# Performance work log

Hardware: AMD Instinct MI355X
Metric: run time of the kernel (lower is better)

Reference implementation:

```python
import jax, jax.numpy as jnp
import numpy as np

B, T, S, PD = 512, 2048, 16, 4

def setup_inputs() -> dict:
    key = jax.random.key(0)
    ks = jax.random.split(key, 10)
    w = lambda k, sh: (jax.random.normal(k, sh, dtype=jnp.float32) * 0.1)
    return {
        'z': jax.random.normal(ks[0], (B, T, S), dtype=jnp.float32),
        'p': jax.random.normal(ks[1], (B, T, PD), dtype=jnp.float32),
        'mu0': jnp.zeros((B, S), dtype=jnp.float32),
        'P0': jnp.full((B, S), 0.1, dtype=jnp.float32),  # cfg['kf_P0']
        'Wq1': w(ks[2], (PD, 64)), 'bq1': jnp.zeros((64,), jnp.float32),
        'Wq2': w(ks[3], (64, S)),  'bq2': jnp.zeros((S,), jnp.float32),
        'Wr1': w(ks[4], (PD, 64)), 'br1': jnp.zeros((64,), jnp.float32),
        'Wr2': w(ks[5], (64, S)),  'br2': jnp.zeros((S,), jnp.float32),
        'Wg1': w(ks[6], (PD, 32)), 'bg1': jnp.zeros((32,), jnp.float32),
        'Wg2': w(ks[7], (32, 1)),  'bg2': jnp.zeros((1,), jnp.float32),
    }

def _mlp(x, W1, b1, W2, b2):
    return jax.nn.relu(x @ W1 + b1) @ W2 + b2

def reference(z, p, mu0, P0, Wq1, bq1, Wq2, bq2, Wr1, br1, Wr2, br2, Wg1, bg1, Wg2, bg2):
    # z: [B,T,S], p: [B,T,PD]; scan over time with batched Kalman state.
    zT = jnp.swapaxes(z, 0, 1)  # [T,B,S]
    pT = jnp.swapaxes(p, 0, 1)  # [T,B,PD]

    def step(carry, inp):
        mu, P = carry            # [B,S], [B,S]
        z_t, p_t = inp           # [B,S], [B,PD]
        Q_t = jax.nn.softplus(_mlp(p_t, Wq1, bq1, Wq2, bq2)) + 1e-8
        R_t = jax.nn.softplus(_mlp(p_t, Wr1, br1, Wr2, br2)) + 1e-8
        P_pred = P + Q_t
        K = jnp.clip(P_pred / (P_pred + R_t), 1e-6, 0.95)
        gamma_t = jax.nn.sigmoid(_mlp(p_t, Wg1, bg1, Wg2, bg2))  # [B,1] (scalar per sample)
        mu_new = mu + gamma_t * (K * (z_t - mu))
        P_new = (1.0 - K) * P_pred
        return (mu_new, P_new), mu_new

    (mu_f, P_f), mus = jax.lax.scan(step, (mu0, P0), (zT, pT))
    return jnp.swapaxes(mus, 0, 1)  # [B,T,S]
```

## Files before the change

kernel.cpp:

```cpp
#include <hip/hip_runtime.h>
#include <hip/hip_fp16.h>
#include <stdint.h>
#include <math.h>

#define KB 512
#define KT 2048
#define KS 16
#define KPD 4

typedef _Float16 f16;
typedef _Float16 f16x4v __attribute__((ext_vector_type(4)));
typedef _Float16 f16x8 __attribute__((ext_vector_type(8)));
typedef float f32x4 __attribute__((ext_vector_type(4)));

#define MFMA16(A, B, C) __builtin_amdgcn_mfma_f32_16x16x32_f16(A, B, C, 0, 0, 0)

__device__ __forceinline__ float softplus_f(float x) {
    float ax = fabsf(x);
    float e  = __expf(-ax);
    return fmaxf(x, 0.0f) + __logf(1.0f + e);
}
__device__ __forceinline__ float sigmoid_f(float x) {
    return __builtin_amdgcn_rcpf(1.0f + __expf(-x));
}
__device__ __forceinline__ float h2f_lo(uint32_t w) {
    return __half2float(__ushort_as_half((unsigned short)(w & 0xffffu)));
}
__device__ __forceinline__ float h2f_hi(uint32_t w) {
    return __half2float(__ushort_as_half((unsigned short)(w >> 16)));
}
__device__ __forceinline__ f16x8 zero8() {
    f16x8 v;
#pragma unroll
    for (int i = 0; i < 8; ++i) v[i] = (f16)0;
    return v;
}

#define HRS 168

__global__ __launch_bounds__(64) void mlp_kernel(
    const float* __restrict__ p,
    const float* __restrict__ Wq1, const float* __restrict__ bq1,
    const float* __restrict__ Wq2, const float* __restrict__ bq2,
    const float* __restrict__ Wr1, const float* __restrict__ br1,
    const float* __restrict__ Wr2, const float* __restrict__ br2,
    const float* __restrict__ Wg1, const float* __restrict__ bg1,
    const float* __restrict__ Wg2, const float* __restrict__ bg2,
    uint32_t* __restrict__ qr_ws, float* __restrict__ g_ws)
{
    __shared__ __align__(16) f16 Hl[2][16][HRS];
    __shared__ __align__(16) f16 Pl[64][4];

    const int l = threadIdx.x;
    const int g = l >> 4;
    const int c = l & 15;
    const int row0 = blockIdx.x * 64;
    const int b = row0 >> 11;
    const int t0 = row0 & (KT - 1);

    f16x8 fA1[10];
#pragma unroll
    for (int m = 0; m < 10; ++m) {
        const float* W = (m < 4) ? (Wq1 + m * 16)
                       : (m < 8) ? (Wr1 + (m - 4) * 16)
                                 : (Wg1 + (m - 8) * 16);
        const int ld = (m < 8) ? 64 : 32;
        float w0 = W[0 * ld + c], w1 = W[1 * ld + c],
              w2 = W[2 * ld + c], w3 = W[3 * ld + c];
        f16x8 a = zero8();
        if (g == 0) { a[0] = (f16)w0; a[1] = (f16)w1; a[2] = (f16)w2; a[3] = (f16)w3; }
        fA1[m] = a;
    }

    f16x8 fA2[5];
#pragma unroll
    for (int i = 0; i < 4; ++i) {
        const float* W = (i < 2) ? Wq2 : Wr2;
        const int kb = (i & 1) * 32;
        f16x8 a;
#pragma unroll
        for (int j = 0; j < 8; ++j) a[j] = (f16)W[(kb + g * 8 + j) * 16 + c];
        fA2[i] = a;
    }
    {
        f16x8 a = zero8();
        if (c == 0) {
#pragma unroll
            for (int j = 0; j < 8; ++j) a[j] = (f16)Wg2[g * 8 + j];
        }
        fA2[4] = a;
    }

    const float bQ0 = bq2[g * 4 + 0], bQ1 = bq2[g * 4 + 1],
                bQ2 = bq2[g * 4 + 2], bQ3 = bq2[g * 4 + 3];
    const float bR0 = br2[g * 4 + 0], bR1 = br2[g * 4 + 1],
                bR2 = br2[g * 4 + 2], bR3 = br2[g * 4 + 3];
    const float bG = bg2[0];

    {
        const float4 pv = *reinterpret_cast<const float4*>(p + (size_t)(row0 + l) * KPD);
        f16x4v v; v[0] = (f16)pv.x; v[1] = (f16)pv.y; v[2] = (f16)pv.z; v[3] = (f16)pv.w;
        *reinterpret_cast<f16x4v*>(&Pl[l][0]) = v;
    }
    asm volatile("s_waitcnt lgkmcnt(0)" ::: "memory");
    __builtin_amdgcn_sched_barrier(0);

    f16x8 fBP[4];
#pragma unroll
    for (int n = 0; n < 4; ++n) {
        f16x8 v = zero8();
        if (g == 0) {
            f16x4v q = *reinterpret_cast<const f16x4v*>(&Pl[n * 16 + c][0]);
            v[0] = q[0]; v[1] = q[1]; v[2] = q[2]; v[3] = q[3];
        }
        fBP[n] = v;
    }

    auto gemm1 = [&](int n, int buf) {
#pragma unroll
        for (int m = 0; m < 10; ++m) {
            const float* bs = (m < 4) ? (bq1 + m * 16)
                            : (m < 8) ? (br1 + (m - 4) * 16)
                                      : (bg1 + (m - 8) * 16);
            f32x4 acc;
            acc[0] = bs[g * 4 + 0]; acc[1] = bs[g * 4 + 1];
            acc[2] = bs[g * 4 + 2]; acc[3] = bs[g * 4 + 3];
            acc = MFMA16(fA1[m], fBP[n], acc);
            auto h01 = __builtin_amdgcn_cvt_pkrtz(fmaxf(acc[0], 0.f), fmaxf(acc[1], 0.f));
            auto h23 = __builtin_amdgcn_cvt_pkrtz(fmaxf(acc[2], 0.f), fmaxf(acc[3], 0.f));
            uint2 w;
            __builtin_memcpy(&w.x, &h01, 4);
            __builtin_memcpy(&w.y, &h23, 4);
            *reinterpret_cast<uint2*>(&Hl[buf][c][m * 16 + g * 4]) = w;
        }
    };

    auto gemm2 = [&](int n, int buf) {
        f16x8 fb0 = *reinterpret_cast<const f16x8*>(&Hl[buf][c][0 * 32 + g * 8]);
        f16x8 fb1 = *reinterpret_cast<const f16x8*>(&Hl[buf][c][1 * 32 + g * 8]);
        f16x8 fb2 = *reinterpret_cast<const f16x8*>(&Hl[buf][c][2 * 32 + g * 8]);
        f16x8 fb3 = *reinterpret_cast<const f16x8*>(&Hl[buf][c][3 * 32 + g * 8]);
        f16x8 fb4 = *reinterpret_cast<const f16x8*>(&Hl[buf][c][4 * 32 + g * 8]);

        f32x4 aq; aq[0] = bQ0; aq[1] = bQ1; aq[2] = bQ2; aq[3] = bQ3;
        aq = MFMA16(fA2[0], fb0, aq);
        aq = MFMA16(fA2[1], fb1, aq);
        f32x4 ar; ar[0] = bR0; ar[1] = bR1; ar[2] = bR2; ar[3] = bR3;
        ar = MFMA16(fA2[2], fb2, ar);
        ar = MFMA16(fA2[3], fb3, ar);
        f32x4 ag; ag[0] = 0.f; ag[1] = 0.f; ag[2] = 0.f; ag[3] = 0.f;
        ag = MFMA16(fA2[4], fb4, ag);

        uint32_t* qdst = qr_ws + ((size_t)b * KS + g * 4) * KT + t0 + n * 16 + c;
#pragma unroll
        for (int i = 0; i < 4; ++i) {
            float Qv = softplus_f(aq[i]) + 1e-8f;
            float Rv = softplus_f(ar[i]) + 1e-8f;
            auto pk = __builtin_amdgcn_cvt_pkrtz(Qv, Rv);
            uint32_t w; __builtin_memcpy(&w, &pk, 4);
            qdst[(size_t)i * KT] = w;
        }
        if (g == 0)
            g_ws[(size_t)b * KT + t0 + n * 16 + c] = sigmoid_f(ag[0] + bG);
    };

    gemm1(0, 0);
#pragma unroll
    for (int n = 0; n < 4; ++n) {
        if (n < 3) gemm1(n + 1, (n + 1) & 1);
        gemm2(n, n & 1);
    }
}

#define QT 512
#define NQ (KT / QT)
#define CL 8

__global__ __launch_bounds__(1024) void scan_kernel(
    const uint32_t* __restrict__ qr_ws, const float* __restrict__ g_ws,
    const float* __restrict__ z, const float* __restrict__ mu0,
    const float* __restrict__ P0, float* __restrict__ out)
{
    __shared__ float smem[QT * 17 + QT];
    float* zmu = smem;
    float* gl  = smem + QT * 17;

    const int b = blockIdx.x;
    const int tid = threadIdx.x;
    const int lane = tid & 63;
    const int s = tid >> 6;

    const uint32_t* qrow = qr_ws + (size_t)(b * KS + s) * KT;
    const float* zb = z + (size_t)b * KT * KS;
    const float* gb = g_ws + (size_t)b * KT;
    float* ob = out + (size_t)b * KT * KS;

    float P_q  = P0[b * KS + s];
    float mu_q = mu0[b * KS + s];

    for (int q = 0; q < NQ; ++q) {
        const int t0 = q * QT;

        {
            const float4* zq = reinterpret_cast<const float4*>(zb + (size_t)t0 * KS);
#pragma unroll
            for (int v = 0; v < 2; ++v) {
                int k = tid * 2 + v;
                float4 w = zq[k];
                int t = k >> 2, s0 = (k & 3) << 2;
                zmu[t * 17 + s0 + 0] = w.x;
                zmu[t * 17 + s0 + 1] = w.y;
                zmu[t * 17 + s0 + 2] = w.z;
                zmu[t * 17 + s0 + 3] = w.w;
            }
            if (tid < QT) gl[tid] = gb[t0 + tid];
        }
        __syncthreads();

        uint32_t qr[CL];
        {
            const uint4* qp = reinterpret_cast<const uint4*>(qrow + t0 + lane * CL);
            uint4 u0 = qp[0], u1 = qp[1];
            qr[0] = u0.x; qr[1] = u0.y; qr[2] = u0.z; qr[3] = u0.w;
            qr[4] = u1.x; qr[5] = u1.y; qr[6] = u1.z; qr[7] = u1.w;
        }
        float c00 = 1.f, c01 = 0.f, c10 = 0.f, c11 = 1.f;
#pragma unroll
        for (int i = 0; i < CL; ++i) {
            float Q = h2f_lo(qr[i]), R = h2f_hi(qr[i]);
            float ta = fmaf(Q, c10, c00);
            float tb = fmaf(Q, c11, c01);
            float n10 = fmaf(Q + R, c10, c00);
            float n11 = fmaf(Q + R, c11, c01);
            c00 = R * ta; c01 = R * tb; c10 = n10; c11 = n11;
        }
        float rn = __builtin_amdgcn_rcpf(c11);
        float ma = c00 * rn, mb = c01 * rn, mc = c10 * rn;

#pragma unroll
        for (int r = 0; r < 6; ++r) {
            const int d = 1 << r;
            float pa = __shfl_up(ma, d);
            float pb = __shfl_up(mb, d);
            float pc = __shfl_up(mc, d);
            float na = fmaf(ma, pa, mb * pc);
            float nb = fmaf(ma, pb, mb);
            float nc = fmaf(mc, pa, pc);
            float nd = fmaf(mc, pb, 1.f);
            float rr = __builtin_amdgcn_rcpf(nd);
            bool act = (lane >= d);
            ma = act ? na * rr : ma;
            mb = act ? nb * rr : mb;
            mc = act ? nc * rr : mc;
        }
        float ea = __shfl_up(ma, 1);
        float eb = __shfl_up(mb, 1);
        float ec = __shfl_up(mc, 1);
        if (lane == 0) { ea = 1.f; eb = 0.f; ec = 0.f; }
        float P = fmaf(ea, P_q, eb) * __builtin_amdgcn_rcpf(fmaf(ec, P_q, 1.f));

        float av[CL], bw[CL];
        float A = 1.f, Bv = 0.f;
#pragma unroll
        for (int i = 0; i < CL; ++i) {
            float Q = h2f_lo(qr[i]), R = h2f_hi(qr[i]);
            float Pp = P + Q;
            float K0 = Pp * __builtin_amdgcn_rcpf(Pp + R);
            float Kk = __builtin_amdgcn_fmed3f(K0, 1e-6f, 0.95f);
            int t = lane * CL + i;
            float g = gl[t];
            float gk = g * Kk;
            float zv = zmu[t * 17 + s];
            av[i] = 1.f - gk;
            bw[i] = gk * zv;
            P = fmaf(-Kk, Pp, Pp);
            A = A * av[i];
            Bv = fmaf(av[i], Bv, bw[i]);
        }
        float P_end = __shfl(P, 63);

#pragma unroll
        for (int r = 0; r < 6; ++r) {
            const int d = 1 << r;
            float pA = __shfl_up(A, d);
            float pB = __shfl_up(Bv, d);
            float nA = A * pA;
            float nB = fmaf(A, pB, Bv);
            bool act = (lane >= d);
            A  = act ? nA : A;
            Bv = act ? nB : Bv;
        }
        float eA = __shfl_up(A, 1);
        float eB = __shfl_up(Bv, 1);
        if (lane == 0) { eA = 1.f; eB = 0.f; }
        float mu = fmaf(eA, mu_q, eB);

        __syncthreads();

#pragma unroll
        for (int i = 0; i < CL; ++i) {
            mu = fmaf(av[i], mu, bw[i]);
            zmu[(lane * CL + i) * 17 + s] = mu;
        }
        float mu_end = __shfl(mu, 63);
        __syncthreads();

#pragma unroll
        for (int v = 0; v < 2; ++v) {
            int k = tid * 2 + v;
            int t = k >> 2, s0 = (k & 3) << 2;
            float4 w;
            w.x = zmu[t * 17 + s0 + 0];
            w.y = zmu[t * 17 + s0 + 1];
            w.z = zmu[t * 17 + s0 + 2];
            w.w = zmu[t * 17 + s0 + 3];
            *reinterpret_cast<float4*>(ob + (size_t)(t0 + t) * KS + s0) = w;
        }
        P_q  = P_end;
        mu_q = mu_end;
        __syncthreads();
    }
}

#define KTT 128
#define KNT (KT / KTT)
#define SROW (KS + 1)

__device__ __forceinline__ void mlp16(const float4 pv,
    const float* __restrict__ W1, const float* __restrict__ b1,
    const float* __restrict__ W2, const float* __restrict__ b2,
    float* __restrict__ acc)
{
#pragma unroll
    for (int j = 0; j < KS; ++j) acc[j] = b2[j];
#pragma unroll 4
    for (int k = 0; k < 64; ++k) {
        float hk = b1[k];
        hk = fmaf(pv.x, W1[k],       hk);
        hk = fmaf(pv.y, W1[64 + k],  hk);
        hk = fmaf(pv.z, W1[128 + k], hk);
        hk = fmaf(pv.w, W1[192 + k], hk);
        hk = fmaxf(hk, 0.0f);
#pragma unroll
        for (int j = 0; j < KS; ++j) acc[j] = fmaf(hk, W2[k * KS + j], acc[j]);
    }
}

__global__ __launch_bounds__(320, 2) void kalman_fused(
    const float* __restrict__ z, const float* __restrict__ p,
    const float* __restrict__ mu0, const float* __restrict__ P0,
    const float* __restrict__ Wq1, const float* __restrict__ bq1,
    const float* __restrict__ Wq2, const float* __restrict__ bq2,
    const float* __restrict__ Wr1, const float* __restrict__ br1,
    const float* __restrict__ Wr2, const float* __restrict__ br2,
    const float* __restrict__ Wg1, const float* __restrict__ bg1,
    const float* __restrict__ Wg2, const float* __restrict__ bg2,
    float* __restrict__ out)
{
    __shared__ float sQ[2][KTT][SROW];
    __shared__ float sR[2][KTT][SROW];
    __shared__ float sZf[2][KTT][KS];
    __shared__ float sGf[2][KTT];

    const int b = blockIdx.x;
    const int tid = threadIdx.x;
    const float* __restrict__ zb = z + (size_t)b * KT * KS;
    const float* __restrict__ pb = p + (size_t)b * KT * KPD;
    float* __restrict__ outb = out + (size_t)b * KT * KS;

    const bool is_mlp = (tid < 256);

    auto do_mlp_tile = [&](int tile, int buf) {
        const int tt = tid & (KTT - 1);
        const int t = tile * KTT + tt;
        const float4 pv = *reinterpret_cast<const float4*>(pb + (size_t)t * KPD);
        float acc[KS];
        if (tid < KTT) {
            mlp16(pv, Wq1, bq1, Wq2, bq2, acc);
#pragma unroll
            for (int j = 0; j < KS; ++j)
                sQ[buf][tt][j] = softplus_f(acc[j]) + 1e-8f;
            float ag = bg2[0];
#pragma unroll 8
            for (int k = 0; k < 32; ++k) {
                float hk = bg1[k];
                hk = fmaf(pv.x, Wg1[k],      hk);
                hk = fmaf(pv.y, Wg1[32 + k], hk);
                hk = fmaf(pv.z, Wg1[64 + k], hk);
                hk = fmaf(pv.w, Wg1[96 + k], hk);
                hk = fmaxf(hk, 0.0f);
                ag = fmaf(hk, Wg2[k], ag);
            }
            sGf[buf][tt] = sigmoid_f(ag);
        } else {
            mlp16(pv, Wr1, br1, Wr2, br2, acc);
#pragma unroll
            for (int j = 0; j < KS; ++j)
                sR[buf][tt][j] = softplus_f(acc[j]) + 1e-8f;
        }
        const float4* __restrict__ zt =
            reinterpret_cast<const float4*>(zb + (size_t)tile * KTT * KS);
        float4* __restrict__ zd = reinterpret_cast<float4*>(&sZf[buf][0][0]);
        zd[tid] = zt[tid];
        zd[tid + 256] = zt[tid + 256];
    };

    float mu = 0.0f, Pv = 0.0f;
    if (!is_mlp) {
        const int lane = tid - 256;
        if (lane < KS) {
            mu = mu0[(size_t)b * KS + lane];
            Pv = P0[(size_t)b * KS + lane];
        }
    }

    if (is_mlp) do_mlp_tile(0, 0);
    __syncthreads();

    for (int k = 0; k < KNT; ++k) {
        const int cur = k & 1;
        if (is_mlp) {
            if (k + 1 < KNT) do_mlp_tile(k + 1, cur ^ 1);
        } else {
            const int lane = tid - 256;
            if (lane < KS) {
                const int s = lane;
                for (int tt = 0; tt < KTT; ++tt) {
                    const float Ppred = Pv + sQ[cur][tt][s];
                    float Kk = Ppred * __builtin_amdgcn_rcpf(Ppred + sR[cur][tt][s]);
                    Kk = __builtin_amdgcn_fmed3f(Kk, 1e-6f, 0.95f);
                    mu = fmaf(sGf[cur][tt] * Kk, sZf[cur][tt][s] - mu, mu);
                    Pv = fmaf(-Kk, Ppred, Ppred);
                    outb[(size_t)(k * KTT + tt) * KS + s] = mu;
                }
            }
        }
        __syncthreads();
    }
}

extern "C" void kernel_launch(void* const* d_in, const int* in_sizes, int n_in,
                              void* d_out, int out_size, void* d_ws, size_t ws_size,
                              hipStream_t stream) {
    const float* z   = (const float*)d_in[0];
    const float* p   = (const float*)d_in[1];
    const float* mu0 = (const float*)d_in[2];
    const float* P0  = (const float*)d_in[3];
    const float* Wq1 = (const float*)d_in[4];
    const float* bq1 = (const float*)d_in[5];
    const float* Wq2 = (const float*)d_in[6];
    const float* bq2 = (const float*)d_in[7];
    const float* Wr1 = (const float*)d_in[8];
    const float* br1 = (const float*)d_in[9];
    const float* Wr2 = (const float*)d_in[10];
    const float* br2 = (const float*)d_in[11];
    const float* Wg1 = (const float*)d_in[12];
    const float* bg1 = (const float*)d_in[13];
    const float* Wg2 = (const float*)d_in[14];
    const float* bg2 = (const float*)d_in[15];
    float* out = (float*)d_out;

    const size_t QR_BYTES = (size_t)KB * KS * KT * 4;
    const size_t G_BYTES  = (size_t)KB * KT * 4;

    if (ws_size >= QR_BYTES + G_BYTES) {
        uint32_t* qr_ws = (uint32_t*)d_ws;
        float* g_ws = (float*)((char*)d_ws + QR_BYTES);
        hipLaunchKernelGGL(mlp_kernel, dim3((KB * KT) / 64), dim3(64), 0, stream,
                           p, Wq1, bq1, Wq2, bq2, Wr1, br1, Wr2, br2,
                           Wg1, bg1, Wg2, bg2, qr_ws, g_ws);
        hipLaunchKernelGGL(scan_kernel, dim3(KB), dim3(1024), 0, stream,
                           qr_ws, g_ws, z, mu0, P0, out);
    } else {
        hipLaunchKernelGGL(kalman_fused, dim3(KB), dim3(320), 0, stream,
                           z, p, mu0, P0, Wq1, bq1, Wq2, bq2,
                           Wr1, br1, Wr2, br2, Wg1, bg1, Wg2, bg2, out);
    }
}
```

Measured before the change: 106.2 us.

## Fuse MFMA MLP and parallel-scan Kalman into one kernel via shared memory

Merges the separate MLP kernel and scan kernel into a single 512-thread kernel per batch. Each quarter of the sequence first has its Q/R/gamma values computed with MFMA and written to LDS, then two scans per wave run over it. This removes the global workspace round trip for Q/R/G (about 70 MB of writes and reads) and one kernel launch. In exchange, the MLP and scan phases are serialized inside each block, each wave now handles two states in sequence, and there are more barriers. The workspace-size fallback path is dropped.

```diff
diff --git a/kernel.cpp b/kernel.cpp
--- a/kernel.cpp
+++ b/kernel.cpp
@@ -7,9 +7,13 @@
 #define KT 2048
 #define KS 16
 #define KPD 4
+#define QT 512
+#define NQ (KT / QT)
+#define NWV 8
+#define HRS 168
+#define QSTR 516
 
 typedef _Float16 f16;
-typedef _Float16 f16x4v __attribute__((ext_vector_type(4)));
 typedef _Float16 f16x8 __attribute__((ext_vector_type(8)));
 typedef float f32x4 __attribute__((ext_vector_type(4)));
 
@@ -36,27 +40,34 @@
     return v;
 }
 
-#define HRS 168
-
-__global__ __launch_bounds__(64) void mlp_kernel(
-    const float* __restrict__ p,
+__global__ __launch_bounds__(512, 4) void kalman_one(
+    const float* __restrict__ z, const float* __restrict__ p,
+    const float* __restrict__ mu0, const float* __restrict__ P0,
     const float* __restrict__ Wq1, const float* __restrict__ bq1,
     const float* __restrict__ Wq2, const float* __restrict__ bq2,
     const float* __restrict__ Wr1, const float* __restrict__ br1,
     const float* __restrict__ Wr2, const float* __restrict__ br2,
     const float* __restrict__ Wg1, const float* __restrict__ bg1,
     const float* __restrict__ Wg2, const float* __restrict__ bg2,
-    uint32_t* __restrict__ qr_ws, float* __restrict__ g_ws)
+    float* __restrict__ out)
 {
-    __shared__ __align__(16) f16 Hl[2][16][HRS];
-    __shared__ __align__(16) f16 Pl[64][4];
-
-    const int l = threadIdx.x;
+    __shared__ __align__(16) uint32_t QRl[KS * QSTR];
+    __shared__ __align__(16) float    Gl[QT];
+    __shared__ __align__(16) uint32_t Ubuf[(NWV * KS * HRS) / 2];
+
+    const int tid = threadIdx.x;
+    const int wv = tid >> 6;
+    const int l = tid & 63;
     const int g = l >> 4;
     const int c = l & 15;
-    const int row0 = blockIdx.x * 64;
-    const int b = row0 >> 11;
-    const int t0 = row0 & (KT - 1);
+    const int b = blockIdx.x;
+
+    f16* __restrict__ Hw = reinterpret_cast<f16*>(Ubuf) + wv * (KS * HRS);
+    float* __restrict__ zmu = reinterpret_cast<float*>(Ubuf);
+
+    const float* __restrict__ zb = z + (size_t)b * KT * KS;
+    const float* __restrict__ pb = p + (size_t)b * KT * KPD;
+    float* __restrict__ ob = out + (size_t)b * KT * KS;
 
     f16x8 fA1[10];
 #pragma unroll
@@ -71,7 +82,6 @@
         if (g == 0) { a[0] = (f16)w0; a[1] = (f16)w1; a[2] = (f16)w2; a[3] = (f16)w3; }
         fA1[m] = a;
     }
-
     f16x8 fA2[5];
 #pragma unroll
     for (int i = 0; i < 4; ++i) {
@@ -90,122 +100,169 @@
         }
         fA2[4] = a;
     }
-
     const float bQ0 = bq2[g * 4 + 0], bQ1 = bq2[g * 4 + 1],
                 bQ2 = bq2[g * 4 + 2], bQ3 = bq2[g * 4 + 3];
     const float bR0 = br2[g * 4 + 0], bR1 = br2[g * 4 + 1],
                 bR2 = br2[g * 4 + 2], bR3 = br2[g * 4 + 3];
     const float bG = bg2[0];
 
-    {
-        const float4 pv = *reinterpret_cast<const float4*>(p + (size_t)(row0 + l) * KPD);
-        f16x4v v; v[0] = (f16)pv.x; v[1] = (f16)pv.y; v[2] = (f16)pv.z; v[3] = (f16)pv.w;
-        *reinterpret_cast<f16x4v*>(&Pl[l][0]) = v;
-    }
-    asm volatile("s_waitcnt lgkmcnt(0)" ::: "memory");
-    __builtin_amdgcn_sched_barrier(0);
-
-    f16x8 fBP[4];
-#pragma unroll
-    for (int n = 0; n < 4; ++n) {
-        f16x8 v = zero8();
-        if (g == 0) {
-            f16x4v q = *reinterpret_cast<const f16x4v*>(&Pl[n * 16 + c][0]);
-            v[0] = q[0]; v[1] = q[1]; v[2] = q[2]; v[3] = q[3];
-        }
-        fBP[n] = v;
-    }
-
-    auto gemm1 = [&](int n, int buf) {
-#pragma unroll
-        for (int m = 0; m < 10; ++m) {
-            const float* bs = (m < 4) ? (bq1 + m * 16)
-                            : (m < 8) ? (br1 + (m - 4) * 16)
-                                      : (bg1 + (m - 8) * 16);
-            f32x4 acc;
-            acc[0] = bs[g * 4 + 0]; acc[1] = bs[g * 4 + 1];
-            acc[2] = bs[g * 4 + 2]; acc[3] = bs[g * 4 + 3];
-            acc = MFMA16(fA1[m], fBP[n], acc);
-            auto h01 = __builtin_amdgcn_cvt_pkrtz(fmaxf(acc[0], 0.f), fmaxf(acc[1], 0.f));
-            auto h23 = __builtin_amdgcn_cvt_pkrtz(fmaxf(acc[2], 0.f), fmaxf(acc[3], 0.f));
-            uint2 w;
-            __builtin_memcpy(&w.x, &h01, 4);
-            __builtin_memcpy(&w.y, &h23, 4);
-            *reinterpret_cast<uint2*>(&Hl[buf][c][m * 16 + g * 4]) = w;
-        }
+    float muA = mu0[b * KS + wv],     PA = P0[b * KS + wv];
+    float muB = mu0[b * KS + wv + 8], PB = P0[b * KS + wv + 8];
+
+    auto scan_s = [&](int s, float& mu_q, float& P_q) {
+        uint32_t qr[8];
+        const uint32_t* qrow = QRl + (size_t)s * QSTR;
+#pragma unroll
+        for (int i = 0; i < 8; ++i) qr[i] = qrow[l * 8 + i];
+        float c00 = 1.f, c01 = 0.f, c10 = 0.f, c11 = 1.f;
+#pragma unroll
+        for (int i = 0; i < 8; ++i) {
+            float Q = h2f_lo(qr[i]), R = h2f_hi(qr[i]);
+            float ta = fmaf(Q, c10, c00);
+            float tb = fmaf(Q, c11, c01);
+            float n10 = fmaf(Q + R, c10, c00);
+            float n11 = fmaf(Q + R, c11, c01);
+            c00 = R * ta; c01 = R * tb; c10 = n10; c11 = n11;
+        }
+        float rn = __builtin_amdgcn_rcpf(c11);
+        float ma = c00 * rn, mb = c01 * rn, mc = c10 * rn;
+#pragma unroll
+        for (int r = 0; r < 6; ++r) {
+            const int d = 1 << r;
+            float pa = __shfl_up(ma, d);
+            float pbv = __shfl_up(mb, d);
+            float pc = __shfl_up(mc, d);
+            float na = fmaf(ma, pa, mb * pc);
+            float nb = fmaf(ma, pbv, mb);
+            float nc = fmaf(mc, pa, pc);
+            float nd = fmaf(mc, pbv, 1.f);
+            float rr = __builtin_amdgcn_rcpf(nd);
+            bool act = (l >= d);
+            ma = act ? na * rr : ma;
+            mb = act ? nb * rr : mb;
+            mc = act ? nc * rr : mc;
+        }
+        float ea = __shfl_up(ma, 1);
+        float eb = __shfl_up(mb, 1);
+        float ec = __shfl_up(mc, 1);
+        if (l == 0) { ea = 1.f; eb = 0.f; ec = 0.f; }
+        float P = fmaf(ea, P_q, eb) * __builtin_amdgcn_rcpf(fmaf(ec, P_q, 1.f));
+
+        float av[8], bw[8];
+        float A = 1.f, Bv = 0.f;
+#pragma unroll
+        for (int i = 0; i < 8; ++i) {
+            float Q = h2f_lo(qr[i]), R = h2f_hi(qr[i]);
+            float Pp = P + Q;
+            float K0 = Pp * __builtin_amdgcn_rcpf(Pp + R);
+            float Kk = __builtin_amdgcn_fmed3f(K0, 1e-6f, 0.95f);
+            int t = l * 8 + i;
+            float gv = Gl[t];
+            float gk = gv * Kk;
+            float zv = zmu[t * 17 + s];
+            av[i] = 1.f - gk;
+            bw[i] = gk * zv;
+            P = fmaf(-Kk, Pp, Pp);
+            A = A * av[i];
+            Bv = fmaf(av[i], Bv, bw[i]);
+        }
+        float P_end = __shfl(P, 63);
+#pragma unroll
+        for (int r = 0; r < 6; ++r) {
+            const int d = 1 << r;
+            float pA = __shfl_up(A, d);
+            float pB = __shfl_up(Bv, d);
+            float nA = A * pA;
+            float nB = fmaf(A, pB, Bv);
+            bool act = (l >= d);
+            A  = act ? nA : A;
+            Bv = act ? nB : Bv;
+        }
+        float eA = __shfl_up(A, 1);
+        float eB = __shfl_up(Bv, 1);
+        if (l == 0) { eA = 1.f; eB = 0.f; }
+        float mu = fmaf(eA, mu_q, eB);
+#pragma unroll
+        for (int i = 0; i < 8; ++i) {
+            mu = fmaf(av[i], mu, bw[i]);
+            zmu[(l * 8 + i) * 17 + s] = mu;
+        }
+        mu_q = __shfl(mu, 63);
+        P_q = P_end;
     };
 
-    auto gemm2 = [&](int n, int buf) {
-        f16x8 fb0 = *reinterpret_cast<const f16x8*>(&Hl[buf][c][0 * 32 + g * 8]);
-        f16x8 fb1 = *reinterpret_cast<const f16x8*>(&Hl[buf][c][1 * 32 + g * 8]);
-        f16x8 fb2 = *reinterpret_cast<const f16x8*>(&Hl[buf][c][2 * 32 + g * 8]);
-        f16x8 fb3 = *reinterpret_cast<const f16x8*>(&Hl[buf][c][3 * 32 + g * 8]);
-        f16x8 fb4 = *reinterpret_cast<const f16x8*>(&Hl[buf][c][4 * 32 + g * 8]);
-
-        f32x4 aq; aq[0] = bQ0; aq[1] = bQ1; aq[2] = bQ2; aq[3] = bQ3;
-        aq = MFMA16(fA2[0], fb0, aq);
-        aq = MFMA16(fA2[1], fb1, aq);
-        f32x4 ar; ar[0] = bR0; ar[1] = bR1; ar[2] = bR2; ar[3] = bR3;
-        ar = MFMA16(fA2[2], fb2, ar);
-        ar = MFMA16(fA2[3], fb3, ar);
-        f32x4 ag; ag[0] = 0.f; ag[1] = 0.f; ag[2] = 0.f; ag[3] = 0.f;
-        ag = MFMA16(fA2[4], fb4, ag);
-
-        uint32_t* qdst = qr_ws + ((size_t)b * KS + g * 4) * KT + t0 + n * 16 + c;
-#pragma unroll
-        for (int i = 0; i < 4; ++i) {
-            float Qv = softplus_f(aq[i]) + 1e-8f;
-            float Rv = softplus_f(ar[i]) + 1e-8f;
-            auto pk = __builtin_amdgcn_cvt_pkrtz(Qv, Rv);
-            uint32_t w; __builtin_memcpy(&w, &pk, 4);
-            qdst[(size_t)i * KT] = w;
-        }
-        if (g == 0)
-            g_ws[(size_t)b * KT + t0 + n * 16 + c] = sigmoid_f(ag[0] + bG);
-    };
-
-    gemm1(0, 0);
-#pragma unroll
-    for (int n = 0; n < 4; ++n) {
-        if (n < 3) gemm1(n + 1, (n + 1) & 1);
-        gemm2(n, n & 1);
-    }
-}
-
-#define QT 512
-#define NQ (KT / QT)
-#define CL 8
-
-__global__ __launch_bounds__(1024) void scan_kernel(
-    const uint32_t* __restrict__ qr_ws, const float* __restrict__ g_ws,
-    const float* __restrict__ z, const float* __restrict__ mu0,
-    const float* __restrict__ P0, float* __restrict__ out)
-{
-    __shared__ float smem[QT * 17 + QT];
-    float* zmu = smem;
-    float* gl  = smem + QT * 17;
-
-    const int b = blockIdx.x;
-    const int tid = threadIdx.x;
-    const int lane = tid & 63;
-    const int s = tid >> 6;
-
-    const uint32_t* qrow = qr_ws + (size_t)(b * KS + s) * KT;
-    const float* zb = z + (size_t)b * KT * KS;
-    const float* gb = g_ws + (size_t)b * KT;
-    float* ob = out + (size_t)b * KT * KS;
-
-    float P_q  = P0[b * KS + s];
-    float mu_q = mu0[b * KS + s];
-
     for (int q = 0; q < NQ; ++q) {
-        const int t0 = q * QT;
-
         {
-            const float4* zq = reinterpret_cast<const float4*>(zb + (size_t)t0 * KS);
-#pragma unroll
-            for (int v = 0; v < 2; ++v) {
-                int k = tid * 2 + v;
+            const int trow = q * QT + wv * 64;
+            const float4 pv = *reinterpret_cast<const float4*>(pb + (size_t)(trow + l) * KPD);
+
+            f16x8 fBP[4];
+#pragma unroll
+            for (int n = 0; n < 4; ++n) {
+                const int src = n * 16 + c;
+                float x = __shfl(pv.x, src);
+                float y = __shfl(pv.y, src);
+                float zz = __shfl(pv.z, src);
+                float w = __shfl(pv.w, src);
+                f16x8 v = zero8();
+                if (g == 0) { v[0] = (f16)x; v[1] = (f16)y; v[2] = (f16)zz; v[3] = (f16)w; }
+                fBP[n] = v;
+            }
+
+#pragma unroll
+            for (int n = 0; n < 4; ++n) {
+#pragma unroll
+                for (int m = 0; m < 10; ++m) {
+                    const float* bs = (m < 4) ? (bq1 + m * 16)
+                                    : (m < 8) ? (br1 + (m - 4) * 16)
+                                              : (bg1 + (m - 8) * 16);
+                    f32x4 acc;
+                    acc[0] = bs[g * 4 + 0]; acc[1] = bs[g * 4 + 1];
+                    acc[2] = bs[g * 4 + 2]; acc[3] = bs[g * 4 + 3];
+                    acc = MFMA16(fA1[m], fBP[n], acc);
+                    auto h01 = __builtin_amdgcn_cvt_pkrtz(fmaxf(acc[0], 0.f), fmaxf(acc[1], 0.f));
+                    auto h23 = __builtin_amdgcn_cvt_pkrtz(fmaxf(acc[2], 0.f), fmaxf(acc[3], 0.f));
+                    uint32_t w0, w1;
+                    __builtin_memcpy(&w0, &h01, 4);
+                    __builtin_memcpy(&w1, &h23, 4);
+                    *reinterpret_cast<uint32_t*>(&Hw[c * HRS + m * 16 + g * 4 + 0]) = w0;
+                    *reinterpret_cast<uint32_t*>(&Hw[c * HRS + m * 16 + g * 4 + 2]) = w1;
+                }
+                f16x8 fb0 = *reinterpret_cast<const f16x8*>(&Hw[c * HRS + 0 * 32 + g * 8]);
+                f16x8 fb1 = *reinterpret_cast<const f16x8*>(&Hw[c * HRS + 1 * 32 + g * 8]);
+                f16x8 fb2 = *reinterpret_cast<const f16x8*>(&Hw[c * HRS + 2 * 32 + g * 8]);
+                f16x8 fb3 = *reinterpret_cast<const f16x8*>(&Hw[c * HRS + 3 * 32 + g * 8]);
+                f16x8 fb4 = *reinterpret_cast<const f16x8*>(&Hw[c * HRS + 4 * 32 + g * 8]);
+
+                f32x4 aq; aq[0] = bQ0; aq[1] = bQ1; aq[2] = bQ2; aq[3] = bQ3;
+                aq = MFMA16(fA2[0], fb0, aq);
+                aq = MFMA16(fA2[1], fb1, aq);
+                f32x4 ar; ar[0] = bR0; ar[1] = bR1; ar[2] = bR2; ar[3] = bR3;
+                ar = MFMA16(fA2[2], fb2, ar);
+                ar = MFMA16(fA2[3], fb3, ar);
+                f32x4 ag; ag[0] = 0.f; ag[1] = 0.f; ag[2] = 0.f; ag[3] = 0.f;
+                ag = MFMA16(fA2[4], fb4, ag);
+
+                uint32_t* qdst = QRl + (size_t)(g * 4) * QSTR + wv * 64 + n * 16 + c;
+#pragma unroll
+                for (int i = 0; i < 4; ++i) {
+                    float Qv = softplus_f(aq[i]) + 1e-8f;
+                    float Rv = softplus_f(ar[i]) + 1e-8f;
+                    auto pk = __builtin_amdgcn_cvt_pkrtz(Qv, Rv);
+                    uint32_t w; __builtin_memcpy(&w, &pk, 4);
+                    qdst[(size_t)i * QSTR] = w;
+                }
+                if (g == 0)
+                    Gl[wv * 64 + n * 16 + c] = sigmoid_f(ag[0] + bG);
+            }
+        }
+        __syncthreads();
+
+        {
+            const float4* zq = reinterpret_cast<const float4*>(zb + (size_t)q * QT * KS);
+#pragma unroll
+            for (int v = 0; v < 4; ++v) {
+                int k = tid + 512 * v;
                 float4 w = zq[k];
                 int t = k >> 2, s0 = (k & 3) << 2;
                 zmu[t * 17 + s0 + 0] = w.x;
@@ -213,226 +270,25 @@
                 zmu[t * 17 + s0 + 2] = w.z;
                 zmu[t * 17 + s0 + 3] = w.w;
             }
-            if (tid < QT) gl[tid] = gb[t0 + tid];
         }
         __syncthreads();
 
-        uint32_t qr[CL];
+        scan_s(wv, muA, PA);
+        scan_s(wv + 8, muB, PB);
+        __syncthreads();
+
         {
-            const uint4* qp = reinterpret_cast<const uint4*>(qrow + t0 + lane * CL);
-            uint4 u0 = qp[0], u1 = qp[1];
-            qr[0] = u0.x; qr[1] = u0.y; qr[2] = u0.z; qr[3] = u0.w;
-            qr[4] = u1.x; qr[5] = u1.y; qr[6] = u1.z; qr[7] = u1.w;
-        }
-        float c00 = 1.f, c01 = 0.f, c10 = 0.f, c11 = 1.f;
-#pragma unroll
-        for (int i = 0; i < CL; ++i) {
-            float Q = h2f_lo(qr[i]), R = h2f_hi(qr[i]);
-            float ta = fmaf(Q, c10, c00);
-            float tb = fmaf(Q, c11, c01);
-            float n10 = fmaf(Q + R, c10, c00);
-            float n11 = fmaf(Q + R, c11, c01);
-            c00 = R * ta; c01 = R * tb; c10 = n10; c11 = n11;
-        }
-        float rn = __builtin_amdgcn_rcpf(c11);
-        float ma = c00 * rn, mb = c01 * rn, mc = c10 * rn;
-
-#pragma unroll
-        for (int r = 0; r < 6; ++r) {
-            const int d = 1 << r;
-            float pa = __shfl_up(ma, d);
-            float pb = __shfl_up(mb, d);
-            float pc = __shfl_up(mc, d);
-            float na = fmaf(ma, pa, mb * pc);
-            float nb = fmaf(ma, pb, mb);
-            float nc = fmaf(mc, pa, pc);
-            float nd = fmaf(mc, pb, 1.f);
-            float rr = __builtin_amdgcn_rcpf(nd);
-            bool act = (lane >= d);
-            ma = act ? na * rr : ma;
-            mb = act ? nb * rr : mb;
-            mc = act ? nc * rr : mc;
-        }
-        float ea = __shfl_up(ma, 1);
-        float eb = __shfl_up(mb, 1);
-        float ec = __shfl_up(mc, 1);
-        if (lane == 0) { ea = 1.f; eb = 0.f; ec = 0.f; }
-        float P = fmaf(ea, P_q, eb) * __builtin_amdgcn_rcpf(fmaf(ec, P_q, 1.f));
-
-        float av[CL], bw[CL];
-        float A = 1.f, Bv = 0.f;
-#pragma unroll
-        for (int i = 0; i < CL; ++i) {
-            float Q = h2f_lo(qr[i]), R = h2f_hi(qr[i]);
-            float Pp = P + Q;
-            float K0 = Pp * __builtin_amdgcn_rcpf(Pp + R);
-            float Kk = __builtin_amdgcn_fmed3f(K0, 1e-6f, 0.95f);
-            int t = lane * CL + i;
-            float g = gl[t];
-            float gk = g * Kk;
-            float zv = zmu[t * 17 + s];
-            av[i] = 1.f - gk;
-            bw[i] = gk * zv;
-            P = fmaf(-Kk, Pp, Pp);
-            A = A * av[i];
-            Bv = fmaf(av[i], Bv, bw[i]);
-        }
-        float P_end = __shfl(P, 63);
-
-#pragma unroll
-        for (int r = 0; r < 6; ++r) {
-            const int d = 1 << r;
-            float pA = __shfl_up(A, d);
-            float pB = __shfl_up(Bv, d);
-            float nA = A * pA;
-            float nB = fmaf(A, pB, Bv);
-            bool act = (lane >= d);
-            A  = act ? nA : A;
-            Bv = act ? nB : Bv;
-        }
-        float eA = __shfl_up(A, 1);
-        float eB = __shfl_up(Bv, 1);
-        if (lane == 0) { eA = 1.f; eB = 0.f; }
-        float mu = fmaf(eA, mu_q, eB);
-
-        __syncthreads();
-
-#pragma unroll
-        for (int i = 0; i < CL; ++i) {
-            mu = fmaf(av[i], mu, bw[i]);
-            zmu[(lane * CL + i) * 17 + s] = mu;
-        }
-        float mu_end = __shfl(mu, 63);
-        __syncthreads();
-
-#pragma unroll
-        for (int v = 0; v < 2; ++v) {
-            int k = tid * 2 + v;
-            int t = k >> 2, s0 = (k & 3) << 2;
-            float4 w;
-            w.x = zmu[t * 17 + s0 + 0];
-            w.y = zmu[t * 17 + s0 + 1];
-            w.z = zmu[t * 17 + s0 + 2];
-            w.w = zmu[t * 17 + s0 + 3];
-            *reinterpret_cast<float4*>(ob + (size_t)(t0 + t) * KS + s0) = w;
-        }
-        P_q  = P_end;
-        mu_q = mu_end;
-        __syncthreads();
-    }
-}
-
-#define KTT 128
-#define KNT (KT / KTT)
-#define SROW (KS + 1)
-
-__device__ __forceinline__ void mlp16(const float4 pv,
-    const float* __restrict__ W1, const float* __restrict__ b1,
-    const float* __restrict__ W2, const float* __restrict__ b2,
-    float* __restrict__ acc)
-{
-#pragma unroll
-    for (int j = 0; j < KS; ++j) acc[j] = b2[j];
-#pragma unroll 4
-    for (int k = 0; k < 64; ++k) {
-        float hk = b1[k];
-        hk = fmaf(pv.x, W1[k],       hk);
-        hk = fmaf(pv.y, W1[64 + k],  hk);
-        hk = fmaf(pv.z, W1[128 + k], hk);
-        hk = fmaf(pv.w, W1[192 + k], hk);
-        hk = fmaxf(hk, 0.0f);
-#pragma unroll
-        for (int j = 0; j < KS; ++j) acc[j] = fmaf(hk, W2[k * KS + j], acc[j]);
-    }
-}
-
-__global__ __launch_bounds__(320, 2) void kalman_fused(
-    const float* __restrict__ z, const float* __restrict__ p,
-    const float* __restrict__ mu0, const float* __restrict__ P0,
-    const float* __restrict__ Wq1, const float* __restrict__ bq1,
-    const float* __restrict__ Wq2, const float* __restrict__ bq2,
-    const float* __restrict__ Wr1, const float* __restrict__ br1,
-    const float* __restrict__ Wr2, const float* __restrict__ br2,
-    const float* __restrict__ Wg1, const float* __restrict__ bg1,
-    const float* __restrict__ Wg2, const float* __restrict__ bg2,
-    float* __restrict__ out)
-{
-    __shared__ float sQ[2][KTT][SROW];
-    __shared__ float sR[2][KTT][SROW];
-    __shared__ float sZf[2][KTT][KS];
-    __shared__ float sGf[2][KTT];
-
-    const int b = blockIdx.x;
-    const int tid = threadIdx.x;
-    const float* __restrict__ zb = z + (size_t)b * KT * KS;
-    const float* __restrict__ pb = p + (size_t)b * KT * KPD;
-    float* __restrict__ outb = out + (size_t)b * KT * KS;
-
-    const bool is_mlp = (tid < 256);
-
-    auto do_mlp_tile = [&](int tile, int buf) {
-        const int tt = tid & (KTT - 1);
-        const int t = tile * KTT + tt;
-        const float4 pv = *reinterpret_cast<const float4*>(pb + (size_t)t * KPD);
-        float acc[KS];
-        if (tid < KTT) {
-            mlp16(pv, Wq1, bq1, Wq2, bq2, acc);
-#pragma unroll
-            for (int j = 0; j < KS; ++j)
-                sQ[buf][tt][j] = softplus_f(acc[j]) + 1e-8f;
-            float ag = bg2[0];
-#pragma unroll 8
-            for (int k = 0; k < 32; ++k) {
-                float hk = bg1[k];
-                hk = fmaf(pv.x, Wg1[k],      hk);
-                hk = fmaf(pv.y, Wg1[32 + k], hk);
-                hk = fmaf(pv.z, Wg1[64 + k], hk);
-                hk = fmaf(pv.w, Wg1[96 + k], hk);
-                hk = fmaxf(hk, 0.0f);
-                ag = fmaf(hk, Wg2[k], ag);
-            }
-            sGf[buf][tt] = sigmoid_f(ag);
-        } else {
-            mlp16(pv, Wr1, br1, Wr2, br2, acc);
-#pragma unroll
-            for (int j = 0; j < KS; ++j)
-                sR[buf][tt][j] = softplus_f(acc[j]) + 1e-8f;
-        }
-        const float4* __restrict__ zt =
-            reinterpret_cast<const float4*>(zb + (size_t)tile * KTT * KS);
-        float4* __restrict__ zd = reinterpret_cast<float4*>(&sZf[buf][0][0]);
-        zd[tid] = zt[tid];
-        zd[tid + 256] = zt[tid + 256];
-    };
-
-    float mu = 0.0f, Pv = 0.0f;
-    if (!is_mlp) {
-        const int lane = tid - 256;
-        if (lane < KS) {
-            mu = mu0[(size_t)b * KS + lane];
-            Pv = P0[(size_t)b * KS + lane];
-        }
-    }
-
-    if (is_mlp) do_mlp_tile(0, 0);
-    __syncthreads();
-
-    for (int k = 0; k < KNT; ++k) {
-        const int cur = k & 1;
-        if (is_mlp) {
-            if (k + 1 < KNT) do_mlp_tile(k + 1, cur ^ 1);
-        } else {
-            const int lane = tid - 256;
-            if (lane < KS) {
-                const int s = lane;
-                for (int tt = 0; tt < KTT; ++tt) {
-                    const float Ppred = Pv + sQ[cur][tt][s];
-                    float Kk = Ppred * __builtin_amdgcn_rcpf(Ppred + sR[cur][tt][s]);
-                    Kk = __builtin_amdgcn_fmed3f(Kk, 1e-6f, 0.95f);
-                    mu = fmaf(sGf[cur][tt] * Kk, sZf[cur][tt][s] - mu, mu);
-                    Pv = fmaf(-Kk, Ppred, Ppred);
-                    outb[(size_t)(k * KTT + tt) * KS + s] = mu;
-                }
+            float* od = ob + (size_t)q * QT * KS;
+#pragma unroll
+            for (int v = 0; v < 4; ++v) {
+                int k = tid + 512 * v;
+                int t = k >> 2, s0 = (k & 3) << 2;
+                float4 w;
+                w.x = zmu[t * 17 + s0 + 0];
+                w.y = zmu[t * 17 + s0 + 1];
+                w.z = zmu[t * 17 + s0 + 2];
+                w.w = zmu[t * 17 + s0 + 3];
+                *reinterpret_cast<float4*>(od + 4 * (size_t)k) = w;
             }
         }
         __syncthreads();
@@ -460,20 +316,7 @@
     const float* bg2 = (const float*)d_in[15];
     float* out = (float*)d_out;
 
-    const size_t QR_BYTES = (size_t)KB * KS * KT * 4;
-    const size_t G_BYTES  = (size_t)KB * KT * 4;
-
-    if (ws_size >= QR_BYTES + G_BYTES) {
-        uint32_t* qr_ws = (uint32_t*)d_ws;
-        float* g_ws = (float*)((char*)d_ws + QR_BYTES);
-        hipLaunchKernelGGL(mlp_kernel, dim3((KB * KT) / 64), dim3(64), 0, stream,
-                           p, Wq1, bq1, Wq2, bq2, Wr1, br1, Wr2, br2,
-                           Wg1, bg1, Wg2, bg2, qr_ws, g_ws);
-        hipLaunchKernelGGL(scan_kernel, dim3(KB), dim3(1024), 0, stream,
-                           qr_ws, g_ws, z, mu0, P0, out);
-    } else {
-        hipLaunchKernelGGL(kalman_fused, dim3(KB), dim3(320), 0, stream,
-                           z, p, mu0, P0, Wq1, bq1, Wq2, bq2,
-                           Wr1, br1, Wr2, br2, Wg1, bg1, Wg2, bg2, out);
-    }
-}
+    hipLaunchKernelGGL(kalman_one, dim3(KB), dim3(512), 0, stream,
+                       z, p, mu0, P0, Wq1, bq1, Wq2, bq2,
+                       Wr1, br1, Wr2, br2, Wg1, bg1, Wg2, bg2, out);
+}
```

After: 153.5 us. +44.5%, slower.
